# Kernel tuning notes

Hardware: AMD Instinct MI355X
Metric: run time of the kernel (lower is better)

## Reference

```python
import jax, jax.numpy as jnp
import numpy as np

HIDDEN = 256
HEADS = 4
HEAD_DIM = HIDDEN // HEADS
SCALE = HEAD_DIM ** -0.5
N1, N2 = 6000, 6000


def setup_inputs() -> dict:
    key = jax.random.key(0)
    ks = jax.random.split(key, 12)
    s = 1.0 / np.sqrt(HIDDEN)
    return {
        "kg1_emb": jax.random.normal(ks[0], (N1, HIDDEN), jnp.float32),
        "kg2_emb": jax.random.normal(ks[1], (N2, HIDDEN), jnp.float32),
        "alignment_matrix": jax.random.bernoulli(ks[2], 0.01, (N1, N2)).astype(jnp.float32),
        "Wq": jax.random.normal(ks[3], (HIDDEN, HIDDEN), jnp.float32) * s,
        "bq": jnp.zeros((HIDDEN,), jnp.float32),
        "Wk": jax.random.normal(ks[4], (HIDDEN, HIDDEN), jnp.float32) * s,
        "bk": jnp.zeros((HIDDEN,), jnp.float32),
        "Wv": jax.random.normal(ks[5], (HIDDEN, HIDDEN), jnp.float32) * s,
        "bv": jnp.zeros((HIDDEN,), jnp.float32),
        "Wo": jax.random.normal(ks[6], (HIDDEN, HIDDEN), jnp.float32) * s,
        "bo": jnp.zeros((HIDDEN,), jnp.float32),
    }


def _cross_attend(q_emb, kv_emb, align, Wq, bq, Wk, bk, Wv, bv):
    # q_emb: [Nq, H*D], kv_emb: [Nk, H*D], align: [Nq, Nk]
    Nq, Nk = q_emb.shape[0], kv_emb.shape[0]
    Q = (q_emb @ Wq.T + bq).reshape(Nq, HEADS, HEAD_DIM)
    K = (kv_emb @ Wk.T + bk).reshape(Nk, HEADS, HEAD_DIM)
    V = (kv_emb @ Wv.T + bv).reshape(Nk, HEADS, HEAD_DIM)
    # einsum('nih,mjh->nmij').mean(-1) == Q against head-mean of K (same math)
    Kbar = K.mean(axis=1)  # [Nk, D]
    scores = jnp.einsum('nid,md->nmi', Q, Kbar) * SCALE  # [Nq, Nk, HEADS]
    scores = scores * align[:, :, None]                  # multiplicative mask
    w = jax.nn.softmax(scores, axis=1)                   # over kv entities
    out = jnp.einsum('nmh,mhd->nhd', w, V)               # [Nq, HEADS, D]
    return out.reshape(Nq, HIDDEN)


def reference(kg1_emb, kg2_emb, alignment_matrix, Wq, bq, Wk, bk, Wv, bv, Wo, bo):
    kg1_from_kg2 = _cross_attend(kg1_emb, kg2_emb, alignment_matrix,
                                 Wq, bq, Wk, bk, Wv, bv)
    kg1_enhanced = kg1_emb + (kg1_from_kg2 @ Wo.T + bo)
    kg2_from_kg1 = _cross_attend(kg2_emb, kg1_emb, alignment_matrix.T,
                                 Wq, bq, Wk, bk, Wv, bv)
    kg2_enhanced = kg2_emb + (kg2_from_kg1 @ Wo.T + bo)
    return (kg1_enhanced, kg2_enhanced)
```

## Files before the change

### kernel.cpp

```cpp
#include <hip/hip_runtime.h>
#include <hip/hip_bf16.h>
#include <stdint.h>

typedef __bf16 bf16_t;
typedef __bf16 bf16x8 __attribute__((ext_vector_type(8)));
typedef __bf16 bf16x4 __attribute__((ext_vector_type(4)));
typedef float f32x4 __attribute__((ext_vector_type(4)));

#define NROW 6000
#define HID 256
#define NHEAD 4
#define HD 64
#define ATT_SCALE 0.125f
#define MTOT 12000
#define CAP 128
#define NCHUNK 4500000

__global__ __launch_bounds__(256)
void canon_w_kernel(const float* __restrict__ wq, const float* __restrict__ wk,
                    const float* __restrict__ wv, const float* __restrict__ wo,
                    bf16_t* __restrict__ cW)
{
    int i = blockIdx.x * 256 + threadIdx.x;
    int seg = i >> 16, k = i & 65535;
    const float* s = (seg == 0) ? wq : (seg == 1) ? wk : (seg == 2) ? wv : wo;
    cW[i] = (bf16_t)s[k];
}

__global__ __launch_bounds__(256)
void proj_qkv_kernel(const float* __restrict__ e1, const float* __restrict__ e2,
                     const bf16_t* __restrict__ cW,
                     const float* __restrict__ bq, const float* __restrict__ bk,
                     const float* __restrict__ bv,
                     bf16_t* __restrict__ Q, bf16_t* __restrict__ Kf, bf16_t* __restrict__ V)
{
    int m0   = blockIdx.x * 64;
    int n0   = blockIdx.y * 64;
    int wave = threadIdx.x >> 6;
    int lane = threadIdx.x & 63;
    int r16  = lane & 15;
    int quad = lane >> 4;

    int sel = n0 >> 8;
    int jb  = n0 & 255;
    const bf16_t* W = cW + (size_t)sel * HID * HID;
    const float* bias = (sel == 0) ? bq : (sel == 1) ? bk : bv;

    int arow = m0 + wave * 16 + r16;
    int rr   = arow < MTOT ? arow : MTOT - 1;
    const float* asrc = (rr < NROW) ? (e1 + (size_t)rr * HID)
                                    : (e2 + (size_t)(rr - NROW) * HID);

    f32x4 acc0 = {0,0,0,0}, acc1 = {0,0,0,0}, acc2 = {0,0,0,0}, acc3 = {0,0,0,0};
#pragma unroll
    for (int kk = 0; kk < HID; kk += 32) {
        f32x4 af0 = *(const f32x4*)(asrc + kk + quad * 8);
        f32x4 af1 = *(const f32x4*)(asrc + kk + quad * 8 + 4);
        bf16x8 a;
#pragma unroll
        for (int i = 0; i < 4; ++i) { a[i] = (bf16_t)af0[i]; a[4 + i] = (bf16_t)af1[i]; }
        const bf16_t* b0 = W + (size_t)(jb + r16) * HID + kk + quad * 8;
        bf16x8 f0 = *(const bf16x8*)(b0);
        bf16x8 f1 = *(const bf16x8*)(b0 + 16 * HID);
        bf16x8 f2 = *(const bf16x8*)(b0 + 32 * HID);
        bf16x8 f3 = *(const bf16x8*)(b0 + 48 * HID);
        acc0 = __builtin_amdgcn_mfma_f32_16x16x32_bf16(a, f0, acc0, 0, 0, 0);
        acc1 = __builtin_amdgcn_mfma_f32_16x16x32_bf16(a, f1, acc1, 0, 0, 0);
        acc2 = __builtin_amdgcn_mfma_f32_16x16x32_bf16(a, f2, acc2, 0, 0, 0);
        acc3 = __builtin_amdgcn_mfma_f32_16x16x32_bf16(a, f3, acc3, 0, 0, 0);
    }
    f32x4 accs[4] = {acc0, acc1, acc2, acc3};
    bf16_t* dst = (sel == 0) ? Q : (sel == 1) ? Kf : V;
    int rbase = m0 + wave * 16 + quad * 4;
#pragma unroll
    for (int nt = 0; nt < 4; ++nt) {
        int j = jb + nt * 16 + r16;
        float bb = bias[j];
#pragma unroll
        for (int rg = 0; rg < 4; ++rg) {
            int r = rbase + rg;
            if (r < MTOT)
                dst[(size_t)r * HID + j] = (bf16_t)(accs[nt][rg] + bb);
        }
    }
}

__global__ __launch_bounds__(256)
void kbar_vsum_kernel(const bf16_t* __restrict__ Kf, const bf16_t* __restrict__ V,
                      bf16_t* __restrict__ Kbar, float* __restrict__ Vsum)
{
    int b = blockIdx.x;
    if (b < 3000) {
        int id = b * 256 + threadIdx.x;
        int m = id >> 6, d = id & 63;
        const bf16_t* kr = Kf + (size_t)m * HID + d;
        Kbar[id] = (bf16_t)(0.25f * ((float)kr[0] + (float)kr[64] +
                                     (float)kr[128] + (float)kr[192]));
    } else {
        int idx = b - 3000;
        int g = idx / 24;
        int seg = idx - g * 24;
        int j = threadIdx.x;
        const bf16_t* base = V + ((size_t)(g * NROW + seg * 250)) * HID + j;
        float s = 0.f;
        for (int m = 0; m < 250; ++m) s += (float)base[(size_t)m * HID];
        atomicAdd(Vsum + g * HID + j, s);
    }
}

__global__ __launch_bounds__(256)
void scan_nz_kernel(const float* __restrict__ am,
                    int* __restrict__ rcur,
                    int* __restrict__ csr)
{
    int lane = threadIdx.x & 63;
    int ch   = blockIdx.x * 256 + threadIdx.x;
    bool oob = (ch >= NCHUNK);
    int che  = oob ? (NCHUNK - 1) : ch;

    unsigned int nzmask = 0;
    if (!oob) {
        const unsigned int* aw = (const unsigned int*)am + (size_t)che * 8;
        uint4 u0 = *(const uint4*)(aw);
        uint4 u1 = *(const uint4*)(aw + 4);
        unsigned int any = u0.x | u0.y | u0.z | u0.w | u1.x | u1.y | u1.z | u1.w;
        if (any) {
            unsigned int w[8] = {u0.x, u0.y, u0.z, u0.w, u1.x, u1.y, u1.z, u1.w};
#pragma unroll
            for (int p = 0; p < 8; ++p)
                if (w[p]) nzmask |= 1u << p;
        }
    }
    int n  = che / 750;
    int m0 = (che - n * 750) * 8;
    int c  = __popc(nzmask);

    int p = c;
#pragma unroll
    for (int off = 1; off < 64; off <<= 1) {
        int t = __shfl_up(p, off);
        if (lane >= off) p += t;
    }
    int excl  = p - c;
    int total = __shfl(p, 63);

    int nFirst = __shfl(n, 0);
    int nLast  = __shfl(n, 63);
    unsigned long long mb = __ballot(n == nLast);
    int s0  = __ffsll(mb) - 1;
    int pS0 = __shfl(excl, s0);

    int baseB = 0;
    if (lane == s0) {
        int totalB = total - pS0;
        if (totalB > 0) baseB = atomicAdd(rcur + nLast, totalB);
    }
    baseB = __shfl(baseB, s0);
    int baseA = 0;
    if (s0 > 0) {
        if (lane == 0 && pS0 > 0) baseA = atomicAdd(rcur + nFirst, pS0);
        baseA = __shfl(baseA, 0);
    }

    int myOff = (n == nLast) ? (baseB + excl - pS0) : (baseA + excl);
    if (c) {
        int* dst = csr + (size_t)n * CAP;
        int w = 0;
#pragma unroll
        for (int pb = 0; pb < 8; ++pb) {
            if (nzmask & (1u << pb)) {
                int idx = myOff + (w++);
                if (idx < CAP) dst[idx] = m0 + pb;
            }
        }
    }
}

__global__ __launch_bounds__(256)
void csc_kernel(const int* __restrict__ rcnt, const int* __restrict__ csr,
                int* __restrict__ ccur, int* __restrict__ csc)
{
    int tid = blockIdx.x * 256 + threadIdx.x;
    int n = tid >> 7, j = tid & (CAP - 1);
    if (n >= NROW) return;
    int cnt = rcnt[n]; if (cnt > CAP) cnt = CAP;
    if (j >= cnt) return;
    int m = csr[(size_t)n * CAP + j];
    int slot = atomicAdd(ccur + m, 1);
    if (slot < CAP) csc[(size_t)m * CAP + slot] = n;
}

__global__ __launch_bounds__(256)
void attn_kernel(const bf16_t* __restrict__ Q, const bf16_t* __restrict__ Kbar,
                 const bf16_t* __restrict__ V, const float* __restrict__ Vsum,
                 const int* __restrict__ rcnt, const int* __restrict__ ccnt,
                 const int* __restrict__ csr, const int* __restrict__ csc,
                 bf16_t* __restrict__ att)
{
    __shared__ __align__(16) bf16_t qsb[HID];
    __shared__ int   ml[CAP];
    __shared__ float sc[CAP * 5];
    __shared__ float w0s[NHEAD];
    __shared__ float red[4 * HID];

    int dir = blockIdx.y;
    int n   = blockIdx.x;
    int t   = threadIdx.x;
    int wave = t >> 6, lane = t & 63;

    size_t qrow = (size_t)(dir ? NROW + n : n);
    const bf16_t* kb_base = Kbar + (dir ? 0 : (size_t)NROW * HD);
    const bf16_t* v_base  = V    + (dir ? 0 : (size_t)NROW * HID);
    const float*  vs      = Vsum + (dir ? 0 : HID);
    const int*    lst     = (dir ? csc : csr) + (size_t)n * CAP;
    int cnt = (dir ? ccnt : rcnt)[n];
    if (cnt > CAP) cnt = CAP;

    qsb[t] = Q[qrow * HID + t];
    for (int j = t; j < cnt; j += 256) ml[j] = lst[j];
    __syncthreads();

    int m16  = lane & 15;
    int quad = lane >> 4;

    {
        bf16x8 b0, b1;
        if (m16 < NHEAD) {
            b0 = *(const bf16x8*)(qsb + m16 * HD + 0  + quad * 8);
            b1 = *(const bf16x8*)(qsb + m16 * HD + 32 + quad * 8);
        } else {
            b0 = (bf16x8)(bf16_t)0.f;
            b1 = (bf16x8)(bf16_t)0.f;
        }
        for (int jt = wave; jt * 16 < cnt; jt += 4) {
            int j  = jt * 16 + m16;
            int jj = j < cnt ? j : cnt - 1;
            int row = ml[jj];
            const bf16_t* ap = kb_base + (size_t)row * HD + quad * 8;
            bf16x8 a0 = *(const bf16x8*)(ap);
            bf16x8 a1 = *(const bf16x8*)(ap + 32);
            f32x4 acc = {0, 0, 0, 0};
            acc = __builtin_amdgcn_mfma_f32_16x16x32_bf16(a0, b0, acc, 0, 0, 0);
            acc = __builtin_amdgcn_mfma_f32_16x16x32_bf16(a1, b1, acc, 0, 0, 0);
            if (m16 < NHEAD) {
#pragma unroll
                for (int rg = 0; rg < 4; ++rg) {
                    int jw = jt * 16 + quad * 4 + rg;
                    if (jw < cnt) sc[jw * 5 + m16] = acc[rg] * ATT_SCALE;
                }
            }
        }
    }
    __syncthreads();

    {
        int head = wave;
        float M = 0.0f;
        for (int j = lane; j < cnt; j += 64) M = fmaxf(M, sc[j * 5 + head]);
        for (int off = 32; off; off >>= 1) M = fmaxf(M, __shfl_xor(M, off));
        float e0 = __expf(-M);
        float e[2]; int k = 0;
        float S = 0.f;
        for (int j = lane; j < cnt; j += 64, ++k) { e[k] = __expf(sc[j * 5 + head] - M); S += e[k]; }
        for (int off = 32; off; off >>= 1) S += __shfl_xor(S, off);
        float Z = S + (float)(NROW - cnt) * e0;
        float invZ = 1.0f / Z;
        k = 0;
        for (int j = lane; j < cnt; j += 64, ++k) sc[j * 5 + head] = (e[k] - e0) * invZ;
        if (lane == 0) w0s[head] = e0 * invZ;
    }
    __syncthreads();

    int h3 = lane >> 4;
    int dq = lane & 15;
    int colb = h3 * HD + dq * 4;
    float a0 = 0.f, a1 = 0.f, a2 = 0.f, a3 = 0.f;
    {
        int j = wave;
        for (; j + 4 < cnt; j += 8) {
            int   m0 = ml[j];            int   m1 = ml[j + 4];
            float c0 = sc[j * 5 + h3];   float c1 = sc[(j + 4) * 5 + h3];
            bf16x4 r0 = *(const bf16x4*)(v_base + (size_t)m0 * HID + colb);
            bf16x4 r1 = *(const bf16x4*)(v_base + (size_t)m1 * HID + colb);
            a0 += c0 * (float)r0[0] + c1 * (float)r1[0];
            a1 += c0 * (float)r0[1] + c1 * (float)r1[1];
            a2 += c0 * (float)r0[2] + c1 * (float)r1[2];
            a3 += c0 * (float)r0[3] + c1 * (float)r1[3];
        }
        if (j < cnt) {
            int   m0 = ml[j];
            float c0 = sc[j * 5 + h3];
            bf16x4 r0 = *(const bf16x4*)(v_base + (size_t)m0 * HID + colb);
            a0 += c0 * (float)r0[0];
            a1 += c0 * (float)r0[1];
            a2 += c0 * (float)r0[2];
            a3 += c0 * (float)r0[3];
        }
    }
    red[wave * 256 + colb + 0] = a0;
    red[wave * 256 + colb + 1] = a1;
    red[wave * 256 + colb + 2] = a2;
    red[wave * 256 + colb + 3] = a3;
    __syncthreads();
    float tot = red[t] + red[256 + t] + red[512 + t] + red[768 + t]
              + w0s[t >> 6] * vs[t];
    att[qrow * HID + t] = (bf16_t)tot;
}

__global__ __launch_bounds__(256)
void proj_out_kernel(const bf16_t* __restrict__ att, const bf16_t* __restrict__ wo,
                     const float* __restrict__ bo,
                     const float* __restrict__ e1, const float* __restrict__ e2,
                     float* __restrict__ out)
{
    int m0   = blockIdx.x * 64;
    int n0   = blockIdx.y * 64;
    int wave = threadIdx.x >> 6;
    int lane = threadIdx.x & 63;
    int r16  = lane & 15;
    int quad = lane >> 4;

    int arow = m0 + wave * 16 + r16;
    int rr   = arow < MTOT ? arow : MTOT - 1;
    const bf16_t* asrc = att + (size_t)rr * HID;

    f32x4 acc0 = {0,0,0,0}, acc1 = {0,0,0,0}, acc2 = {0,0,0,0}, acc3 = {0,0,0,0};
#pragma unroll
    for (int kk = 0; kk < HID; kk += 32) {
        bf16x8 a = *(const bf16x8*)(asrc + kk + quad * 8);
        const bf16_t* b0 = wo + (size_t)(n0 + r16) * HID + kk + quad * 8;
        bf16x8 f0 = *(const bf16x8*)(b0);
        bf16x8 f1 = *(const bf16x8*)(b0 + 16 * HID);
        bf16x8 f2 = *(const bf16x8*)(b0 + 32 * HID);
        bf16x8 f3 = *(const bf16x8*)(b0 + 48 * HID);
        acc0 = __builtin_amdgcn_mfma_f32_16x16x32_bf16(a, f0, acc0, 0, 0, 0);
        acc1 = __builtin_amdgcn_mfma_f32_16x16x32_bf16(a, f1, acc1, 0, 0, 0);
        acc2 = __builtin_amdgcn_mfma_f32_16x16x32_bf16(a, f2, acc2, 0, 0, 0);
        acc3 = __builtin_amdgcn_mfma_f32_16x16x32_bf16(a, f3, acc3, 0, 0, 0);
    }
    f32x4 accs[4] = {acc0, acc1, acc2, acc3};
    int rbase = m0 + wave * 16 + quad * 4;
#pragma unroll
    for (int nt = 0; nt < 4; ++nt) {
        int j = n0 + nt * 16 + r16;
        float bb = bo[j];
#pragma unroll
        for (int rg = 0; rg < 4; ++rg) {
            int r = rbase + rg;
            if (r < MTOT) {
                const float* emb = (r < NROW) ? (e1 + (size_t)r * HID)
                                              : (e2 + (size_t)(r - NROW) * HID);
                float v = accs[nt][rg] + bb + emb[j];
                out[(size_t)r * HID + j] = v;
            }
        }
    }
}

extern "C" void kernel_launch(void* const* d_in, const int* in_sizes, int n_in,
                              void* d_out, int out_size, void* d_ws, size_t ws_size,
                              hipStream_t stream)
{
    const float* e1 = (const float*)d_in[0];
    const float* e2 = (const float*)d_in[1];
    const float* am = (const float*)d_in[2];
    const float* wq = (const float*)d_in[3];
    const float* bq = (const float*)d_in[4];
    const float* wk = (const float*)d_in[5];
    const float* bk = (const float*)d_in[6];
    const float* wv = (const float*)d_in[7];
    const float* bv = (const float*)d_in[8];
    const float* wo = (const float*)d_in[9];
    const float* bo = (const float*)d_in[10];
    float* out = (float*)d_out;

    size_t off = 0;
    char* base = (char*)d_ws;
    auto alloc = [&](size_t bytes) -> void* {
        void* p = base + off;
        off += (bytes + 255) & ~(size_t)255;
        return p;
    };
    bf16_t* Q    = (bf16_t*)alloc((size_t)MTOT * HID * 2);
    bf16_t* Kf   = (bf16_t*)alloc((size_t)MTOT * HID * 2);
    bf16_t* V    = (bf16_t*)alloc((size_t)MTOT * HID * 2);
    bf16_t* Kbar = (bf16_t*)alloc((size_t)MTOT * HD * 2);
    bf16_t* att  = (bf16_t*)alloc((size_t)MTOT * HID * 2);
    bf16_t* cW   = (bf16_t*)alloc((size_t)4 * HID * HID * 2);
    int*    csr  = (int*)   alloc((size_t)NROW * CAP * 4);
    int*    csc  = (int*)   alloc((size_t)NROW * CAP * 4);
    int*    rcur = (int*)   alloc(NROW * 4);
    int*    ccur = (int*)   alloc(NROW * 4);
    float*  Vsum = (float*) alloc(2 * HID * 4);

    size_t zero_bytes = (size_t)((char*)Vsum - (char*)rcur) + 2 * HID * 4;
    hipMemsetAsync(rcur, 0, zero_bytes, stream);

    canon_w_kernel<<<1024, 256, 0, stream>>>(wq, wk, wv, wo, cW);

    proj_qkv_kernel<<<dim3(188, 12), 256, 0, stream>>>(
        e1, e2, cW, bq, bk, bv, Q, Kf, V);

    kbar_vsum_kernel<<<3048, 256, 0, stream>>>(Kf, V, Kbar, Vsum);

    scan_nz_kernel<<<(NCHUNK + 255) / 256, 256, 0, stream>>>(am, rcur, csr);
    csc_kernel<<<(NROW * CAP) / 256, 256, 0, stream>>>(rcur, csr, ccur, csc);

    attn_kernel<<<dim3(NROW, 2), 256, 0, stream>>>(
        Q, Kbar, V, Vsum, rcur, ccur, csr, csc, att);

    proj_out_kernel<<<dim3(188, 4), 256, 0, stream>>>(att, cW + 3 * HID * HID, bo, e1, e2, out);
}
```

Before: 387.0 us.

## Merge independent kernels into combined launches and widen mask scan chunks

Puts the weight-cast kernel and the alignment-mask nonzero scan into one grid, and the QKV projection and CSC transpose into another, picking the role by block index. This drops two launches and lets independent work share the GPU instead of running one after the other. The mask scan also reads 16 floats per thread instead of 8, which halves the thread count. In exchange, the blocks of a merged grid are unevenly loaded, and the QKV projection grid is flattened from 2D to 1D.

Result: faster. 373.4 us (-3.5%).

```diff
diff --git a/kernel.cpp b/kernel.cpp
--- a/kernel.cpp
+++ b/kernel.cpp
@@ -14,28 +14,115 @@
 #define ATT_SCALE 0.125f
 #define MTOT 12000
 #define CAP 128
-#define NCHUNK 4500000
+#define NCH16 2250000
+
+#define CANON_BLOCKS 1024
+#define SCAN_BLOCKS  ((NCH16 + 255) / 256)
+#define PROJ_BLOCKS  (188 * 12)
+#define CSC_BLOCKS   ((NROW * CAP) / 256)
 
 __global__ __launch_bounds__(256)
-void canon_w_kernel(const float* __restrict__ wq, const float* __restrict__ wk,
-                    const float* __restrict__ wv, const float* __restrict__ wo,
-                    bf16_t* __restrict__ cW)
-{
-    int i = blockIdx.x * 256 + threadIdx.x;
-    int seg = i >> 16, k = i & 65535;
-    const float* s = (seg == 0) ? wq : (seg == 1) ? wk : (seg == 2) ? wv : wo;
-    cW[i] = (bf16_t)s[k];
+void l1_canon_scan(const float* __restrict__ wq, const float* __restrict__ wk,
+                   const float* __restrict__ wv, const float* __restrict__ wo,
+                   bf16_t* __restrict__ cW,
+                   const float* __restrict__ am,
+                   int* __restrict__ rcur,
+                   int* __restrict__ csr)
+{
+    if (blockIdx.x < CANON_BLOCKS) {
+        int i = blockIdx.x * 256 + threadIdx.x;
+        int seg = i >> 16, k = i & 65535;
+        const float* s = (seg == 0) ? wq : (seg == 1) ? wk : (seg == 2) ? wv : wo;
+        cW[i] = (bf16_t)s[k];
+        return;
+    }
+    int lane = threadIdx.x & 63;
+    int ch   = (blockIdx.x - CANON_BLOCKS) * 256 + threadIdx.x;
+    bool oob = (ch >= NCH16);
+    int che  = oob ? (NCH16 - 1) : ch;
+
+    unsigned int nzmask = 0;
+    if (!oob) {
+        const uint4* p4 = (const uint4*)((const unsigned int*)am + (size_t)che * 16);
+        uint4 u0 = p4[0], u1 = p4[1], u2 = p4[2], u3 = p4[3];
+        unsigned int any = u0.x | u0.y | u0.z | u0.w | u1.x | u1.y | u1.z | u1.w
+                         | u2.x | u2.y | u2.z | u2.w | u3.x | u3.y | u3.z | u3.w;
+        if (any) {
+            unsigned int w[16] = {u0.x, u0.y, u0.z, u0.w, u1.x, u1.y, u1.z, u1.w,
+                                  u2.x, u2.y, u2.z, u2.w, u3.x, u3.y, u3.z, u3.w};
+#pragma unroll
+            for (int p = 0; p < 16; ++p)
+                if (w[p]) nzmask |= 1u << p;
+        }
+    }
+    int n  = che / 375;
+    int m0 = (che - n * 375) * 16;
+    int c  = __popc(nzmask);
+
+    int p = c;
+#pragma unroll
+    for (int off = 1; off < 64; off <<= 1) {
+        int t = __shfl_up(p, off);
+        if (lane >= off) p += t;
+    }
+    int excl  = p - c;
+    int total = __shfl(p, 63);
+
+    int nFirst = __shfl(n, 0);
+    int nLast  = __shfl(n, 63);
+    unsigned long long mb = __ballot(n == nLast);
+    int s0  = __ffsll(mb) - 1;
+    int pS0 = __shfl(excl, s0);
+
+    int baseB = 0;
+    if (lane == s0) {
+        int totalB = total - pS0;
+        if (totalB > 0) baseB = atomicAdd(rcur + nLast, totalB);
+    }
+    baseB = __shfl(baseB, s0);
+    int baseA = 0;
+    if (s0 > 0) {
+        if (lane == 0 && pS0 > 0) baseA = atomicAdd(rcur + nFirst, pS0);
+        baseA = __shfl(baseA, 0);
+    }
+
+    int myOff = (n == nLast) ? (baseB + excl - pS0) : (baseA + excl);
+    if (c) {
+        int* dst = csr + (size_t)n * CAP;
+        int w = 0;
+#pragma unroll
+        for (int pb = 0; pb < 16; ++pb) {
+            if (nzmask & (1u << pb)) {
+                int idx = myOff + (w++);
+                if (idx < CAP) dst[idx] = m0 + pb;
+            }
+        }
+    }
 }
 
 __global__ __launch_bounds__(256)
-void proj_qkv_kernel(const float* __restrict__ e1, const float* __restrict__ e2,
-                     const bf16_t* __restrict__ cW,
-                     const float* __restrict__ bq, const float* __restrict__ bk,
-                     const float* __restrict__ bv,
-                     bf16_t* __restrict__ Q, bf16_t* __restrict__ Kf, bf16_t* __restrict__ V)
-{
-    int m0   = blockIdx.x * 64;
-    int n0   = blockIdx.y * 64;
+void l2_proj_csc(const float* __restrict__ e1, const float* __restrict__ e2,
+                 const bf16_t* __restrict__ cW,
+                 const float* __restrict__ bq, const float* __restrict__ bk,
+                 const float* __restrict__ bv,
+                 bf16_t* __restrict__ Q, bf16_t* __restrict__ Kf, bf16_t* __restrict__ V,
+                 const int* __restrict__ rcnt, const int* __restrict__ csr,
+                 int* __restrict__ ccur, int* __restrict__ csc)
+{
+    if (blockIdx.x >= PROJ_BLOCKS) {
+        int tid = (blockIdx.x - PROJ_BLOCKS) * 256 + threadIdx.x;
+        int n = tid >> 7, j = tid & (CAP - 1);
+        if (n >= NROW) return;
+        int cnt = rcnt[n]; if (cnt > CAP) cnt = CAP;
+        if (j >= cnt) return;
+        int m = csr[(size_t)n * CAP + j];
+        int slot = atomicAdd(ccur + m, 1);
+        if (slot < CAP) csc[(size_t)m * CAP + slot] = n;
+        return;
+    }
+    int bx   = blockIdx.x;
+    int m0   = (bx % 188) * 64;
+    int n0   = (bx / 188) * 64;
     int wave = threadIdx.x >> 6;
     int lane = threadIdx.x & 63;
     int r16  = lane & 15;
@@ -106,88 +193,6 @@
         for (int m = 0; m < 250; ++m) s += (float)base[(size_t)m * HID];
         atomicAdd(Vsum + g * HID + j, s);
     }
-}
-
-__global__ __launch_bounds__(256)
-void scan_nz_kernel(const float* __restrict__ am,
-                    int* __restrict__ rcur,
-                    int* __restrict__ csr)
-{
-    int lane = threadIdx.x & 63;
-    int ch   = blockIdx.x * 256 + threadIdx.x;
-    bool oob = (ch >= NCHUNK);
-    int che  = oob ? (NCHUNK - 1) : ch;
-
-    unsigned int nzmask = 0;
-    if (!oob) {
-        const unsigned int* aw = (const unsigned int*)am + (size_t)che * 8;
-        uint4 u0 = *(const uint4*)(aw);
-        uint4 u1 = *(const uint4*)(aw + 4);
-        unsigned int any = u0.x | u0.y | u0.z | u0.w | u1.x | u1.y | u1.z | u1.w;
-        if (any) {
-            unsigned int w[8] = {u0.x, u0.y, u0.z, u0.w, u1.x, u1.y, u1.z, u1.w};
-#pragma unroll
-            for (int p = 0; p < 8; ++p)
-                if (w[p]) nzmask |= 1u << p;
-        }
-    }
-    int n  = che / 750;
-    int m0 = (che - n * 750) * 8;
-    int c  = __popc(nzmask);
-
-    int p = c;
-#pragma unroll
-    for (int off = 1; off < 64; off <<= 1) {
-        int t = __shfl_up(p, off);
-        if (lane >= off) p += t;
-    }
-    int excl  = p - c;
-    int total = __shfl(p, 63);
-
-    int nFirst = __shfl(n, 0);
-    int nLast  = __shfl(n, 63);
-    unsigned long long mb = __ballot(n == nLast);
-    int s0  = __ffsll(mb) - 1;
-    int pS0 = __shfl(excl, s0);
-
-    int baseB = 0;
-    if (lane == s0) {
-        int totalB = total - pS0;
-        if (totalB > 0) baseB = atomicAdd(rcur + nLast, totalB);
-    }
-    baseB = __shfl(baseB, s0);
-    int baseA = 0;
-    if (s0 > 0) {
-        if (lane == 0 && pS0 > 0) baseA = atomicAdd(rcur + nFirst, pS0);
-        baseA = __shfl(baseA, 0);
-    }
-
-    int myOff = (n == nLast) ? (baseB + excl - pS0) : (baseA + excl);
-    if (c) {
-        int* dst = csr + (size_t)n * CAP;
-        int w = 0;
-#pragma unroll
-        for (int pb = 0; pb < 8; ++pb) {
-            if (nzmask & (1u << pb)) {
-                int idx = myOff + (w++);
-                if (idx < CAP) dst[idx] = m0 + pb;
-            }
-        }
-    }
-}
-
-__global__ __launch_bounds__(256)
-void csc_kernel(const int* __restrict__ rcnt, const int* __restrict__ csr,
-                int* __restrict__ ccur, int* __restrict__ csc)
-{
-    int tid = blockIdx.x * 256 + threadIdx.x;
-    int n = tid >> 7, j = tid & (CAP - 1);
-    if (n >= NROW) return;
-    int cnt = rcnt[n]; if (cnt > CAP) cnt = CAP;
-    if (j >= cnt) return;
-    int m = csr[(size_t)n * CAP + j];
-    int slot = atomicAdd(ccur + m, 1);
-    if (slot < CAP) csc[(size_t)m * CAP + slot] = n;
 }
 
 __global__ __launch_bounds__(256)
@@ -396,18 +401,17 @@
     size_t zero_bytes = (size_t)((char*)Vsum - (char*)rcur) + 2 * HID * 4;
     hipMemsetAsync(rcur, 0, zero_bytes, stream);
 
-    canon_w_kernel<<<1024, 256, 0, stream>>>(wq, wk, wv, wo, cW);
-
-    proj_qkv_kernel<<<dim3(188, 12), 256, 0, stream>>>(
-        e1, e2, cW, bq, bk, bv, Q, Kf, V);
+    l1_canon_scan<<<CANON_BLOCKS + SCAN_BLOCKS, 256, 0, stream>>>(
+        wq, wk, wv, wo, cW, am, rcur, csr);
+
+    l2_proj_csc<<<PROJ_BLOCKS + CSC_BLOCKS, 256, 0, stream>>>(
+        e1, e2, cW, bq, bk, bv, Q, Kf, V, rcur, csr, ccur, csc);
 
     kbar_vsum_kernel<<<3048, 256, 0, stream>>>(Kf, V, Kbar, Vsum);
-
-    scan_nz_kernel<<<(NCHUNK + 255) / 256, 256, 0, stream>>>(am, rcur, csr);
-    csc_kernel<<<(NROW * CAP) / 256, 256, 0, stream>>>(rcur, csr, ccur, csc);
 
     attn_kernel<<<dim3(NROW, 2), 256, 0, stream>>>(
         Q, Kbar, V, Vsum, rcur, ccur, csr, csc, att);
 
-    proj_out_kernel<<<dim3(188, 4), 256, 0, stream>>>(att, cW + 3 * HID * HID, bo, e1, e2, out);
-}
+    proj_out_kernel<<<dim3(188, 4), 256, 0, stream>>>(
+        att, cW + 3 * HID * HID, bo, e1, e2, out);
+}
```
